# Optimization experiments

Hardware: AMD Instinct MI355X
Metric: run time of the kernel (lower is better)

## Reference

```python
import jax, jax.numpy as jnp
import numpy as np

EPS_NORM = 1e-12
EPS_ENT = 1e-12
TEMPERATURE = 0.5
CONTRAST_DENOM = 128.0 * 100.0


def _l2_normalize(x, axis=-1):
    n = jnp.linalg.norm(x, axis=axis, keepdims=True)
    return x / jnp.maximum(n, EPS_NORM)


def setup_inputs() -> dict:
    key0 = jax.random.key(0)
    k1, k2, k3, k4 = jax.random.split(key0, 4)
    B, L, C = 16, 2048, 512
    M = 512
    return {
        "key": jax.random.normal(k1, (B, L, C), dtype=jnp.float32),
        "query": jax.random.normal(k2, (B, L, C), dtype=jnp.float32),
        "keys": jax.random.uniform(k3, (M, C), dtype=jnp.float32),
        "values": jax.random.uniform(k4, (M, C), dtype=jnp.float32),
        "mode": 0,
    }


def reference(key, query, keys, values, mode):
    B, L, C = key.shape
    k = _l2_normalize(key.reshape(-1, C))    # [T, C]
    q = _l2_normalize(query.reshape(-1, C))  # [T, C]

    # --- gatheringLoss ---
    score = jnp.einsum('tc,mc->tm', k, keys)            # [T, M]
    # top-1 of softmax(score) == argmax(score) (softmax is monotone)
    idx = jnp.argmax(score, axis=1)                     # [T]
    nearest_values = values[idx]                        # [T, C]
    gathering_loss = jnp.mean((q - nearest_values) ** 2)

    logits = score / TEMPERATURE                        # [T, M]
    logp = jax.nn.log_softmax(logits, axis=-1)
    gathered = jnp.take_along_axis(logp, idx[:, None], axis=1)  # [T, 1]
    contrast_loss = jnp.sum(gathered) / (-CONTRAST_DENOM)

    # --- read ---
    weights = jax.nn.softmax(score, axis=-1)            # [T, M]
    # EntropyLoss: mean over rows of -sum(w * log(w + eps))
    entropy_loss = jnp.mean(-jnp.sum(weights * jnp.log(weights + EPS_ENT), axis=-1))
    read_query = weights @ values                       # [T, C]

    return (read_query.reshape(B, L, C), entropy_loss, gathering_loss,
            contrast_loss, keys, values)
```

## Files before the change

kernel.cpp:

```cpp
#include <hip/hip_runtime.h>

typedef short short8 __attribute__((ext_vector_type(8)));
typedef float floatx4 __attribute__((ext_vector_type(4)));

#define C_DIM 512
#define KQ_STRIDE 1040

__device__ __forceinline__ unsigned short f2bf(float f) {
    unsigned u = __builtin_bit_cast(unsigned, f);
    u = u + 0x7fffu + ((u >> 16) & 1u);
    return (unsigned short)(u >> 16);
}

__device__ __forceinline__ unsigned skey(float s, int col) {
    unsigned u = __builtin_bit_cast(unsigned, s);
    u = ((int)u < 0) ? ~u : (u | 0x80000000u);
    return (u & ~0x1FFu) | (unsigned)(511 - col);
}

__global__ __launch_bounds__(256) void pack_kernel(
    const float* __restrict__ keys, const float* __restrict__ values,
    unsigned short* __restrict__ keysFrag, unsigned short* __restrict__ valsFrag,
    float* __restrict__ keysOut, float* __restrict__ valsOut,
    float* __restrict__ scal) {
    int tid = blockIdx.x * 256 + threadIdx.x;
    if (tid < 65536) {
        int e  = tid & 32767;
        int l  = e & 63;
        int NT = (e >> 6) & 31;
        int kt = e >> 11;
        int li = l & 15, q4 = l >> 4;
        unsigned short tmp[8];
        if (tid < 32768) {
            const float* s = keys + (size_t)(NT * 16 + li) * C_DIM + kt * 32 + q4 * 8;
#pragma unroll
            for (int j = 0; j < 8; j++) tmp[j] = f2bf(s[j]);
            unsigned short* d = keysFrag + ((size_t)(kt * 32 + NT) * 64 + l) * 8;
            *(ushort4*)d       = make_ushort4(tmp[0], tmp[1], tmp[2], tmp[3]);
            *(ushort4*)(d + 4) = make_ushort4(tmp[4], tmp[5], tmp[6], tmp[7]);
        } else {
#pragma unroll
            for (int j = 0; j < 8; j++)
                tmp[j] = f2bf(values[(size_t)(kt * 32 + q4 * 8 + j) * C_DIM + NT * 16 + li]);
            unsigned short* d = valsFrag + ((size_t)(kt * 32 + NT) * 64 + l) * 8;
            *(ushort4*)d       = make_ushort4(tmp[0], tmp[1], tmp[2], tmp[3]);
            *(ushort4*)(d + 4) = make_ushort4(tmp[4], tmp[5], tmp[6], tmp[7]);
        }
    } else {
        int ct = tid - 65536;
        if (ct == 0) { scal[0] = 0.f; scal[1] = 0.f; scal[2] = 0.f; }
#pragma unroll
        for (int i = 0; i < 4; i++) {
            int idx = ct + i * 32768;
            if (idx < 65536) ((float4*)keysOut)[idx] = ((const float4*)keys)[idx];
            else             ((float4*)valsOut)[idx - 65536] = ((const float4*)values)[idx - 65536];
        }
    }
}

__global__ __launch_bounds__(512, 4) void fused_kernel(
    const float* __restrict__ key,
    const float* __restrict__ query,
    const unsigned short* __restrict__ keysFrag,
    const unsigned short* __restrict__ valsFrag,
    const float* __restrict__ values,
    float* __restrict__ outRQ,
    float* __restrict__ scal) {
    __shared__ char kq[64 * KQ_STRIDE];
    __shared__ __align__(16) float stats[8][64][4];
    __shared__ float gpart[8];

    const int tid = threadIdx.x;
    const int w  = tid >> 6;
    const int l  = tid & 63;
    const int li = l & 15;
    const int q4 = l >> 4;
    const int row0 = blockIdx.x << 6;

#pragma unroll
    for (int it = 0; it < 2; it++) {
        int r = (w << 3) + (it << 2) + q4;
        const float4* src = (const float4*)(key + (size_t)(row0 + r) * C_DIM);
        float4 v[8];
        float ss = 0.f;
#pragma unroll
        for (int i = 0; i < 8; i++) {
            v[i] = src[i * 16 + li];
            ss += v[i].x * v[i].x + v[i].y * v[i].y + v[i].z * v[i].z + v[i].w * v[i].w;
        }
#pragma unroll
        for (int m = 1; m < 16; m <<= 1) ss += __shfl_xor(ss, m, 64);
        float inv = 1.0f / fmaxf(sqrtf(ss), 1e-12f);
        char* dstrow = kq + r * KQ_STRIDE;
#pragma unroll
        for (int i = 0; i < 8; i++) {
            ushort4 b = make_ushort4(f2bf(v[i].x * inv), f2bf(v[i].y * inv),
                                     f2bf(v[i].z * inv), f2bf(v[i].w * inv));
            *(ushort4*)(dstrow + i * 128 + li * 8) = b;
        }
    }
    __syncthreads();

    floatx4 acc1[16];
#pragma unroll
    for (int i = 0; i < 16; i++) acc1[i] = (floatx4){0.f, 0.f, 0.f, 0.f};
    {
        const short8* kf = (const short8*)keysFrag;
        short8 bcur[4], bnxt[4];
#pragma unroll
        for (int nt = 0; nt < 4; nt++) bcur[nt] = kf[(size_t)((w * 4 + nt) * 64 + l)];
        for (int kt = 0; kt < 16; kt++) {
            if (kt < 15) {
#pragma unroll
                for (int nt = 0; nt < 4; nt++)
                    bnxt[nt] = kf[(size_t)(((kt + 1) * 32 + w * 4 + nt) * 64 + l)];
            }
            short8 a[4];
#pragma unroll
            for (int rg = 0; rg < 4; rg++)
                a[rg] = *(const short8*)(kq + (rg * 16 + li) * KQ_STRIDE + kt * 64 + q4 * 16);
#pragma unroll
            for (int rg = 0; rg < 4; rg++)
#pragma unroll
                for (int nt = 0; nt < 4; nt++)
                    acc1[rg * 4 + nt] = __builtin_amdgcn_mfma_f32_16x16x32_bf16(
                        a[rg], bcur[nt], acc1[rg * 4 + nt], 0, 0, 0);
#pragma unroll
            for (int nt = 0; nt < 4; nt++) bcur[nt] = bnxt[nt];
        }
    }

#pragma unroll
    for (int rg = 0; rg < 4; rg++) {
#pragma unroll
        for (int reg = 0; reg < 4; reg++) {
            const int colbase = (w << 6) + li;
            float s0 = acc1[rg * 4 + 0][reg];
            float s1 = acc1[rg * 4 + 1][reg];
            float s2 = acc1[rg * 4 + 2][reg];
            float s3 = acc1[rg * 4 + 3][reg];
            unsigned K  = skey(s0, colbase);
            unsigned K1 = skey(s1, colbase + 16);
            unsigned K2 = skey(s2, colbase + 32);
            unsigned K3 = skey(s3, colbase + 48);
            K = K1 > K ? K1 : K;
            K = K2 > K ? K2 : K;
            K = K3 > K ? K3 : K;
            float p0 = __expf(s0), p1 = __expf(s1), p2 = __expf(s2), p3 = __expf(s3);
            float z1 = (p0 + p1) + (p2 + p3);
            float e1 = p0 * s0 + p1 * s1 + p2 * s2 + p3 * s3;
            float z2 = p0 * p0 + p1 * p1 + p2 * p2 + p3 * p3;
            acc1[rg * 4 + 0][reg] = p0;
            acc1[rg * 4 + 1][reg] = p1;
            acc1[rg * 4 + 2][reg] = p2;
            acc1[rg * 4 + 3][reg] = p3;
#pragma unroll
            for (int msk = 1; msk < 16; msk <<= 1) {
                unsigned Ko = __shfl_xor(K, msk, 64);
                z1 += __shfl_xor(z1, msk, 64);
                e1 += __shfl_xor(e1, msk, 64);
                z2 += __shfl_xor(z2, msk, 64);
                K = Ko > K ? Ko : K;
            }
            if (li == 0) {
                floatx4 sv;
                sv[0] = __builtin_bit_cast(float, K);
                sv[1] = z1; sv[2] = e1; sv[3] = z2;
                *(floatx4*)stats[w][rg * 16 + q4 * 4 + reg] = sv;
            }
        }
    }
    __syncthreads();

#pragma unroll
    for (int rg = 0; rg < 4; rg++) {
#pragma unroll
        for (int reg = 0; reg < 4; reg++) {
            int r = rg * 16 + q4 * 4 + reg;
#pragma unroll
            for (int nt = 0; nt < 4; nt++) {
                int col = (w << 6) + nt * 16 + li;
                *(unsigned short*)(kq + r * KQ_STRIDE + col * 2) = f2bf(acc1[rg * 4 + nt][reg]);
            }
        }
    }
    __syncthreads();

    floatx4 acc2[16];
#pragma unroll
    for (int i = 0; i < 16; i++) acc2[i] = (floatx4){0.f, 0.f, 0.f, 0.f};
    {
        const short8* vf = (const short8*)valsFrag;
        short8 bcur[4], bnxt[4];
#pragma unroll
        for (int nt = 0; nt < 4; nt++) bcur[nt] = vf[(size_t)((w * 4 + nt) * 64 + l)];
        for (int kt = 0; kt < 16; kt++) {
            if (kt < 15) {
#pragma unroll
                for (int nt = 0; nt < 4; nt++)
                    bnxt[nt] = vf[(size_t)(((kt + 1) * 32 + w * 4 + nt) * 64 + l)];
            }
            short8 a[4];
#pragma unroll
            for (int rg = 0; rg < 4; rg++)
                a[rg] = *(const short8*)(kq + (rg * 16 + li) * KQ_STRIDE + kt * 64 + q4 * 16);
#pragma unroll
            for (int rg = 0; rg < 4; rg++)
#pragma unroll
                for (int nt = 0; nt < 4; nt++)
                    acc2[rg * 4 + nt] = __builtin_amdgcn_mfma_f32_16x16x32_bf16(
                        a[rg], bcur[nt], acc2[rg * 4 + nt], 0, 0, 0);
#pragma unroll
            for (int nt = 0; nt < 4; nt++) bcur[nt] = bnxt[nt];
        }
    }

    unsigned K; float z1, e1, z2;
    {
        floatx4 v = *(const floatx4*)stats[0][l];
        K = __builtin_bit_cast(unsigned, v[0]); z1 = v[1]; e1 = v[2]; z2 = v[3];
#pragma unroll
        for (int p = 1; p < 8; p++) {
            floatx4 u = *(const floatx4*)stats[p][l];
            unsigned Ko = __builtin_bit_cast(unsigned, u[0]);
            K = Ko > K ? Ko : K;
            z1 += u[1]; e1 += u[2]; z2 += u[3];
        }
    }
    const float iz = 1.0f / z1;
    const int myidx = 511 - (int)(K & 0x1FFu);

#pragma unroll
    for (int rg = 0; rg < 4; rg++) {
#pragma unroll
        for (int reg = 0; reg < 4; reg++) {
            int r = rg * 16 + q4 * 4 + reg;
            float izr = __shfl(iz, r, 64);
            float* orow = outRQ + (size_t)(row0 + r) * C_DIM + (w << 6) + li;
#pragma unroll
            for (int nt = 0; nt < 4; nt++) orow[nt * 16] = acc2[rg * 4 + nt][reg] * izr;
        }
    }

    float gacc = 0.f;
#pragma unroll
    for (int rr = 0; rr < 8; rr++) {
        int r = (w << 3) + rr;
        int idxr = __shfl(myidx, r, 64);
        const float4* qr = (const float4*)(query + (size_t)(row0 + r) * C_DIM);
        float4 a = qr[l * 2], b = qr[l * 2 + 1];
        float ss = a.x * a.x + a.y * a.y + a.z * a.z + a.w * a.w +
                   b.x * b.x + b.y * b.y + b.z * b.z + b.w * b.w;
#pragma unroll
        for (int m = 1; m < 64; m <<= 1) ss += __shfl_xor(ss, m, 64);
        float inv = 1.0f / fmaxf(sqrtf(ss), 1e-12f);
        const float4* vr = (const float4*)(values + (size_t)idxr * C_DIM);
        float4 va = vr[l * 2], vb = vr[l * 2 + 1];
        float d;
        d = a.x * inv - va.x; gacc += d * d;
        d = a.y * inv - va.y; gacc += d * d;
        d = a.z * inv - va.z; gacc += d * d;
        d = a.w * inv - va.w; gacc += d * d;
        d = b.x * inv - vb.x; gacc += d * d;
        d = b.y * inv - vb.y; gacc += d * d;
        d = b.z * inv - vb.z; gacc += d * d;
        d = b.w * inv - vb.w; gacc += d * d;
    }
#pragma unroll
    for (int m = 1; m < 64; m <<= 1) gacc += __shfl_xor(gacc, m, 64);
    if (l == 0) gpart[w] = gacc;

    if (w == 0) {
        unsigned um = (K >> 31) ? (K & 0x7FFFFFFFu) : ~K;
        um &= ~0x1FFu;
        float m1 = __builtin_bit_cast(float, um);
        float ent = __logf(z1) - e1 * iz;
        float con = __logf(z2) - 2.0f * m1;
#pragma unroll
        for (int msk = 1; msk < 64; msk <<= 1) {
            ent += __shfl_xor(ent, msk, 64);
            con += __shfl_xor(con, msk, 64);
        }
        if (l == 0) {
            atomicAdd(&scal[0], ent * (1.0f / 32768.0f));
            atomicAdd(&scal[2], con * (1.0f / 12800.0f));
        }
    }
    __syncthreads();
    if (tid == 0) {
        float s = 0.f;
#pragma unroll
        for (int i = 0; i < 8; i++) s += gpart[i];
        atomicAdd(&scal[1], s * (1.0f / (32768.0f * 512.0f)));
    }
}

extern "C" void kernel_launch(void* const* d_in, const int* in_sizes, int n_in,
                              void* d_out, int out_size, void* d_ws, size_t ws_size,
                              hipStream_t stream) {
    (void)in_sizes; (void)n_in; (void)out_size; (void)ws_size;
    const float* key    = (const float*)d_in[0];
    const float* query  = (const float*)d_in[1];
    const float* keysIn = (const float*)d_in[2];
    const float* valsIn = (const float*)d_in[3];
    float* out = (float*)d_out;

    unsigned short* keysFrag = (unsigned short*)d_ws;
    unsigned short* valsFrag = keysFrag + 512 * 512;

    float* outRQ   = out;
    float* scal    = out + 16777216;
    float* keysOut = out + 16777219;
    float* valsOut = keysOut + 262144;

    pack_kernel<<<384, 256, 0, stream>>>(keysIn, valsIn, keysFrag, valsFrag,
                                         keysOut, valsOut, scal);
    fused_kernel<<<512, 512, 0, stream>>>(key, query, keysFrag, valsFrag, valsIn, outRQ, scal);
}
```

Before: 245.1 us.

## Halve rows per block to 32 and stage output through LDS for coalesced stores

Each block now handles 32 rows instead of 64, which doubles the grid to 1024 blocks, halves the accumulator registers and LDS per block, and raises launch_bounds occupancy from 4 to 6. The read_query output is staged through shared memory so it can be written as float4 rows instead of scattered scalar stores. In exchange, each B fragment loaded from keysFrag/valsFrag is reused across fewer rows, so global/L2 traffic for those fragments doubles. Per-row stats reductions are adjusted for the 32-row layout, and an extra barrier is added.

Result: slower. 285.9 us (+16.7%).

```diff
diff --git a/kernel.cpp b/kernel.cpp
--- a/kernel.cpp
+++ b/kernel.cpp
@@ -5,6 +5,7 @@
 
 #define C_DIM 512
 #define KQ_STRIDE 1040
+#define ROWS 32
 
 __device__ __forceinline__ unsigned short f2bf(float f) {
     unsigned u = __builtin_bit_cast(unsigned, f);
@@ -58,7 +59,7 @@
     }
 }
 
-__global__ __launch_bounds__(512, 4) void fused_kernel(
+__global__ __launch_bounds__(512, 6) void fused_kernel(
     const float* __restrict__ key,
     const float* __restrict__ query,
     const unsigned short* __restrict__ keysFrag,
@@ -66,8 +67,8 @@
     const float* __restrict__ values,
     float* __restrict__ outRQ,
     float* __restrict__ scal) {
-    __shared__ char kq[64 * KQ_STRIDE];
-    __shared__ __align__(16) float stats[8][64][4];
+    __shared__ char kq[ROWS * KQ_STRIDE];
+    __shared__ __align__(16) float stats[8][ROWS][4];
     __shared__ float gpart[8];
 
     const int tid = threadIdx.x;
@@ -75,11 +76,10 @@
     const int l  = tid & 63;
     const int li = l & 15;
     const int q4 = l >> 4;
-    const int row0 = blockIdx.x << 6;
-
-#pragma unroll
-    for (int it = 0; it < 2; it++) {
-        int r = (w << 3) + (it << 2) + q4;
+    const int row0 = blockIdx.x << 5;
+
+    {
+        int r = (w << 2) + q4;
         const float4* src = (const float4*)(key + (size_t)(row0 + r) * C_DIM);
         float4 v[8];
         float ss = 0.f;
@@ -101,9 +101,9 @@
     }
     __syncthreads();
 
-    floatx4 acc1[16];
-#pragma unroll
-    for (int i = 0; i < 16; i++) acc1[i] = (floatx4){0.f, 0.f, 0.f, 0.f};
+    floatx4 acc1[8];
+#pragma unroll
+    for (int i = 0; i < 8; i++) acc1[i] = (floatx4){0.f, 0.f, 0.f, 0.f};
     {
         const short8* kf = (const short8*)keysFrag;
         short8 bcur[4], bnxt[4];
@@ -115,12 +115,12 @@
                 for (int nt = 0; nt < 4; nt++)
                     bnxt[nt] = kf[(size_t)(((kt + 1) * 32 + w * 4 + nt) * 64 + l)];
             }
-            short8 a[4];
-#pragma unroll
-            for (int rg = 0; rg < 4; rg++)
+            short8 a[2];
+#pragma unroll
+            for (int rg = 0; rg < 2; rg++)
                 a[rg] = *(const short8*)(kq + (rg * 16 + li) * KQ_STRIDE + kt * 64 + q4 * 16);
 #pragma unroll
-            for (int rg = 0; rg < 4; rg++)
+            for (int rg = 0; rg < 2; rg++)
 #pragma unroll
                 for (int nt = 0; nt < 4; nt++)
                     acc1[rg * 4 + nt] = __builtin_amdgcn_mfma_f32_16x16x32_bf16(
@@ -131,7 +131,7 @@
     }
 
 #pragma unroll
-    for (int rg = 0; rg < 4; rg++) {
+    for (int rg = 0; rg < 2; rg++) {
 #pragma unroll
         for (int reg = 0; reg < 4; reg++) {
             const int colbase = (w << 6) + li;
@@ -173,7 +173,7 @@
     __syncthreads();
 
 #pragma unroll
-    for (int rg = 0; rg < 4; rg++) {
+    for (int rg = 0; rg < 2; rg++) {
 #pragma unroll
         for (int reg = 0; reg < 4; reg++) {
             int r = rg * 16 + q4 * 4 + reg;
@@ -186,9 +186,9 @@
     }
     __syncthreads();
 
-    floatx4 acc2[16];
-#pragma unroll
-    for (int i = 0; i < 16; i++) acc2[i] = (floatx4){0.f, 0.f, 0.f, 0.f};
+    floatx4 acc2[8];
+#pragma unroll
+    for (int i = 0; i < 8; i++) acc2[i] = (floatx4){0.f, 0.f, 0.f, 0.f};
     {
         const short8* vf = (const short8*)valsFrag;
         short8 bcur[4], bnxt[4];
@@ -200,12 +200,12 @@
                 for (int nt = 0; nt < 4; nt++)
                     bnxt[nt] = vf[(size_t)(((kt + 1) * 32 + w * 4 + nt) * 64 + l)];
             }
-            short8 a[4];
-#pragma unroll
-            for (int rg = 0; rg < 4; rg++)
+            short8 a[2];
+#pragma unroll
+            for (int rg = 0; rg < 2; rg++)
                 a[rg] = *(const short8*)(kq + (rg * 16 + li) * KQ_STRIDE + kt * 64 + q4 * 16);
 #pragma unroll
-            for (int rg = 0; rg < 4; rg++)
+            for (int rg = 0; rg < 2; rg++)
 #pragma unroll
                 for (int nt = 0; nt < 4; nt++)
                     acc2[rg * 4 + nt] = __builtin_amdgcn_mfma_f32_16x16x32_bf16(
@@ -217,11 +217,12 @@
 
     unsigned K; float z1, e1, z2;
     {
-        floatx4 v = *(const floatx4*)stats[0][l];
+        const int lr = l & 31;
+        floatx4 v = *(const floatx4*)stats[0][lr];
         K = __builtin_bit_cast(unsigned, v[0]); z1 = v[1]; e1 = v[2]; z2 = v[3];
 #pragma unroll
         for (int p = 1; p < 8; p++) {
-            floatx4 u = *(const floatx4*)stats[p][l];
+            floatx4 u = *(const floatx4*)stats[p][lr];
             unsigned Ko = __builtin_bit_cast(unsigned, u[0]);
             K = Ko > K ? Ko : K;
             z1 += u[1]; e1 += u[2]; z2 += u[3];
@@ -230,22 +231,33 @@
     const float iz = 1.0f / z1;
     const int myidx = 511 - (int)(K & 0x1FFu);
 
-#pragma unroll
-    for (int rg = 0; rg < 4; rg++) {
-#pragma unroll
-        for (int reg = 0; reg < 4; reg++) {
-            int r = rg * 16 + q4 * 4 + reg;
-            float izr = __shfl(iz, r, 64);
-            float* orow = outRQ + (size_t)(row0 + r) * C_DIM + (w << 6) + li;
-#pragma unroll
-            for (int nt = 0; nt < 4; nt++) orow[nt * 16] = acc2[rg * 4 + nt][reg] * izr;
+    __syncthreads();
+
+    {
+        float* ws = (float*)kq + w * 1024;
+#pragma unroll
+        for (int rg = 0; rg < 2; rg++) {
+#pragma unroll
+            for (int reg = 0; reg < 4; reg++) {
+                int lr = q4 * 4 + reg;
+                float izr = __shfl(iz, rg * 16 + lr, 64);
+#pragma unroll
+                for (int nt = 0; nt < 4; nt++)
+                    ws[lr * 64 + nt * 16 + li] = acc2[rg * 4 + nt][reg] * izr;
+            }
+#pragma unroll
+            for (int j = 0; j < 4; j++) {
+                int lr = j * 4 + q4;
+                float4 val = *(const float4*)&ws[lr * 64 + li * 4];
+                *(float4*)(outRQ + (size_t)(row0 + rg * 16 + lr) * C_DIM + (w << 6) + li * 4) = val;
+            }
         }
     }
 
     float gacc = 0.f;
 #pragma unroll
-    for (int rr = 0; rr < 8; rr++) {
-        int r = (w << 3) + rr;
+    for (int rr = 0; rr < 4; rr++) {
+        int r = (w << 2) + rr;
         int idxr = __shfl(myidx, r, 64);
         const float4* qr = (const float4*)(query + (size_t)(row0 + r) * C_DIM);
         float4 a = qr[l * 2], b = qr[l * 2 + 1];
@@ -277,7 +289,7 @@
         float ent = __logf(z1) - e1 * iz;
         float con = __logf(z2) - 2.0f * m1;
 #pragma unroll
-        for (int msk = 1; msk < 64; msk <<= 1) {
+        for (int msk = 1; msk < 32; msk <<= 1) {
             ent += __shfl_xor(ent, msk, 64);
             con += __shfl_xor(con, msk, 64);
         }
@@ -315,5 +327,5 @@
 
     pack_kernel<<<384, 256, 0, stream>>>(keysIn, valsIn, keysFrag, valsFrag,
                                          keysOut, valsOut, scal);
-    fused_kernel<<<512, 512, 0, stream>>>(key, query, keysFrag, valsFrag, valsIn, outRQ, scal);
-}
+    fused_kernel<<<1024, 512, 0, stream>>>(key, query, keysFrag, valsFrag, valsIn, outRQ, scal);
+}
```
